# Kernel tuning notes

Measured on AMD Instinct MI355X. Metric: run time of the kernel, lower is better.

Reference implementation:

```python
import jax, jax.numpy as jnp
import numpy as np

B, S, IN, H, D, NH, L, C = 32, 512, 3, 64, 128, 8, 4, 5
NSUB = 10          # euler substeps per interval: dt = interval/10 for these inputs
MAX_CONSEC = 50    # max_consecutive_steps in torch code
DH = D // NH
EPS = 1e-5


def _ln(x, g, b):
    m = x.mean(-1, keepdims=True)
    v = ((x - m) ** 2).mean(-1, keepdims=True)
    return (x - m) / jnp.sqrt(v + EPS) * g + b


def setup_inputs():
    key = jax.random.key(0)
    ks = jax.random.split(key, 24)
    def g(i, shape, scale=0.05):
        return jax.random.normal(ks[i], shape, dtype=jnp.float32) * scale
    dts = jax.random.uniform(ks[0], (B, S), minval=0.001, maxval=0.05, dtype=jnp.float32)
    times = jnp.cumsum(dts, axis=1)  # strictly increasing, positive
    return dict(
        time_series=jax.random.normal(ks[1], (B, S, IN), dtype=jnp.float32),
        times=times,
        noise=jax.random.normal(ks[2], (S, NSUB, B, H), dtype=jnp.float32),
        mask=jnp.ones((B, S), dtype=bool),
        enc_w=g(3, (IN, H)), enc_b=jnp.zeros((H,)),
        enc_g=jnp.ones((H,)), enc_beta=jnp.zeros((H,)),
        dw1=g(4, (H + 1, 2 * H)), db1=jnp.zeros((2 * H,)),
        dw2=g(5, (2 * H, H)), db2=jnp.zeros((H,)),
        dw3=g(6, (H, H)), db3=jnp.zeros((H,)),
        aw1=g(7, (1, H)), ab1=jnp.zeros((H,)),
        aw2=g(8, (H, H)), ab2=jnp.zeros((H,)),
        bw1=g(9, (1, H)), bb1=jnp.zeros((H,)),
        bw2=g(10, (H, H)), bb2=jnp.zeros((H,)),
        min_diff=jnp.float32(0.1),
        in_w=g(11, (H, D)), in_b=jnp.zeros((D,)),
        wq=g(12, (L, D, D)), bq=jnp.zeros((L, D)),
        wk=g(13, (L, D, D)), bk=jnp.zeros((L, D)),
        wv=g(14, (L, D, D)), bv=jnp.zeros((L, D)),
        wo=g(15, (L, D, D)), bo=jnp.zeros((L, D)),
        ln1_g=jnp.ones((L, D)), ln1_b=jnp.zeros((L, D)),
        ln2_g=jnp.ones((L, D)), ln2_b=jnp.zeros((L, D)),
        fw1=g(16, (L, D, 4 * D)), fb1=jnp.zeros((L, 4 * D)),
        fw2=g(17, (L, 4 * D, D)), fb2=jnp.zeros((L, D)),
        cw1=g(18, (D, D // 2)), cb1=jnp.zeros((D // 2,)),
        cw2=g(19, (D // 2, C)), cb2=jnp.zeros((C,)),
    )


def reference(time_series, times, noise, mask, enc_w, enc_b, enc_g, enc_beta,
              dw1, db1, dw2, db2, dw3, db3, aw1, ab1, aw2, ab2, bw1, bb1, bw2, bb2,
              min_diff, in_w, in_b, wq, bq, wk, bk, wv, bv, wo, bo,
              ln1_g, ln1_b, ln2_g, ln2_b, fw1, fb1, fw2, fb2, cw1, cb1, cw2, cb2):
    # feature encoder: Linear -> LayerNorm -> ReLU (dropout off / eval)
    enc = jax.nn.relu(_ln(time_series @ enc_w + enc_b, enc_g, enc_beta))  # (B,S,H)

    def drift(t, y):
        tcol = jnp.full((y.shape[0], 1), t, dtype=y.dtype)
        ty = jnp.concatenate([y, tcol], axis=1)
        h1 = jnp.tanh(ty @ dw1 + db1)
        h2 = jnp.tanh(h1 @ dw2 + db2)
        return h2 @ dw3 + db3

    def diffusion(t, y):
        tcol = jnp.full((y.shape[0], 1), t, dtype=y.dtype)
        A = jax.nn.softplus(jnp.tanh(tcol @ aw1 + ab1) @ aw2 + ab2)
        Bt = jnp.tanh(jnp.tanh(tcol @ bw1 + bb1) @ bw2 + bb2)
        return A + Bt * y + jnp.abs(min_diff)

    t_seq = times[0]  # torch code uses batch element 0's timestamps for sdeint

    def step(carry, xs):
        state, consec = carry
        enc_i, t_prev, t_cur, dW = xs  # dW: (NSUB,B,H) standard normals
        h = (t_cur - t_prev) / NSUB    # dt = interval/10 (< self.dt for these inputs)
        sqh = jnp.sqrt(h)
        y0 = jax.lax.stop_gradient(state)  # torch detaches y0 at every step

        def sub(y, kw):
            k, dw = kw
            t = t_prev + k * h
            return y + drift(t, y) * h + diffusion(t, y) * sqh * dw, None

        y_int, _ = jax.lax.scan(sub, y0, (jnp.arange(NSUB, dtype=jnp.float32), dW))
        skip = consec >= MAX_CONSEC
        out = jnp.where(skip, enc_i, y_int)
        consec = jnp.where(skip, jnp.int32(0), consec + 1)
        return (out, consec), out

    y0 = enc[:, 0]
    xs = (jnp.swapaxes(enc, 0, 1)[1:], t_seq[:-1], t_seq[1:], noise[1:])
    _, traj = jax.lax.scan(step, (y0, jnp.int32(0)), xs)
    sde_features = jnp.concatenate([y0[:, None], jnp.swapaxes(traj, 0, 1)], axis=1)  # (B,S,H)

    mf = mask.astype(sde_features.dtype)
    sde_features = sde_features * mf[..., None]  # MaskedSequenceProcessor.apply_mask

    # ContiFormer (post-LN transformer encoder) over SDE features
    x = sde_features @ in_w + in_b  # (B,S,D)
    neg = jnp.asarray(-1e9, x.dtype)
    for l in range(L):
        q = (x @ wq[l] + bq[l]).reshape(B, S, NH, DH)
        k = (x @ wk[l] + bk[l]).reshape(B, S, NH, DH)
        v = (x @ wv[l] + bv[l]).reshape(B, S, NH, DH)
        scores = jnp.einsum('bqhd,bkhd->bhqk', q, k) / np.float32(np.sqrt(DH))
        scores = jnp.where(mask[:, None, None, :], scores, neg)
        att = jax.nn.softmax(scores, axis=-1)
        o = jnp.einsum('bhqk,bkhd->bqhd', att, v).reshape(B, S, D) @ wo[l] + bo[l]
        x = _ln(x + o, ln1_g[l], ln1_b[l])
        f = jax.nn.relu(x @ fw1[l] + fb1[l]) @ fw2[l] + fb2[l]
        x = _ln(x + f, ln2_g[l], ln2_b[l])
    pooled = (x * mf[..., None]).sum(1) / jnp.maximum(mf.sum(1, keepdims=True), 1.0)

    logits = jax.nn.relu(pooled @ cw1 + cb1) @ cw2 + cb2
    return logits, sde_features
```

## Files before the change

### kernel.cpp

```cpp
#include <hip/hip_runtime.h>
#include <hip/hip_bf16.h>


typedef __attribute__((ext_vector_type(8))) short short8;
typedef __attribute__((ext_vector_type(4))) float f32x4;

static constexpr int OFF_TS      = 0;
static constexpr int OFF_TIMES   = 49152;
static constexpr int OFF_ENCW    = 65536;
static constexpr int OFF_ENCB    = 65728;
static constexpr int OFF_ENCG    = 65792;
static constexpr int OFF_ENCBETA = 65856;
static constexpr int OFF_DW1     = 65920;
static constexpr int OFF_DB1     = 74240;
static constexpr int OFF_DW2     = 74368;
static constexpr int OFF_DB2     = 82560;
static constexpr int OFF_DW3     = 82624;
static constexpr int OFF_DB3     = 86720;
static constexpr int OFF_AW1     = 86784;
static constexpr int OFF_AB1     = 86848;
static constexpr int OFF_AW2     = 86912;
static constexpr int OFF_AB2     = 91008;
static constexpr int OFF_BW1     = 91072;
static constexpr int OFF_BB1     = 91136;
static constexpr int OFF_BW2     = 91200;
static constexpr int OFF_BB2     = 95296;
static constexpr int OFF_MD      = 95360;
static constexpr int OFF_INW     = 95424;
static constexpr int OFF_INB     = 103616;
static constexpr int OFF_WQ      = 103744;
static constexpr int OFF_BQ      = 169280;
static constexpr int OFF_WK      = 169792;
static constexpr int OFF_BK      = 235328;
static constexpr int OFF_WV      = 235840;
static constexpr int OFF_BV      = 301376;
static constexpr int OFF_WO      = 301888;
static constexpr int OFF_BO      = 367424;
static constexpr int OFF_LN1G    = 367936;
static constexpr int OFF_LN1B    = 368448;
static constexpr int OFF_LN2G    = 368960;
static constexpr int OFF_LN2B    = 369472;
static constexpr int OFF_FW1     = 369984;
static constexpr int OFF_FB1     = 632128;
static constexpr int OFF_FW2     = 634176;
static constexpr int OFF_FB2     = 896320;
static constexpr int OFF_CW1     = 896832;
static constexpr int OFF_CB1     = 905024;
static constexpr int OFF_CW2     = 905088;
static constexpr int OFF_CB2     = 905472;
static constexpr int OFF_FLAG    = 905536;
static constexpr int OFF_ENC     = 905600;
static constexpr int OFF_COEFA   = 3002752;
static constexpr int OFF_COEFB   = 3329792;
static constexpr int OFF_B1C     = 3656832;
// ... 278 lines not shown
        c0 = __builtin_amdgcn_mfma_f32_16x16x32_bf16(a0, B1f[0][0], c0, 0, 0, 0);
        c0 = __builtin_amdgcn_mfma_f32_16x16x32_bf16(a1, B1f[1][0], c0, 0, 0, 0);
        f32x4 c1 = {bias_b, bias_b, bias_b, bias_b};
        c1 = __builtin_amdgcn_mfma_f32_16x16x32_bf16(a0, B1f[0][1], c1, 0, 0, 0);
        c1 = __builtin_amdgcn_mfma_f32_16x16x32_bf16(a1, B1f[1][1], c1, 0, 0, 0);
#pragma unroll
        for (int r = 0; r < 4; ++r) {
          h1bf[(q*4 + r)*136 + w*32 + lq]      = f2bf(tanh5(c0[r]));
          h1bf[(q*4 + r)*136 + w*32 + 16 + lq] = f2bf(tanh5(c1[r]));
        }
      }
      lds_barrier();
      {
        short8 h0 = *(const short8*)&h1bf[lq*136 + q*8];
        short8 h1 = *(const short8*)&h1bf[lq*136 + 32 + q*8];
        short8 h2 = *(const short8*)&h1bf[lq*136 + 64 + q*8];
        short8 h3 = *(const short8*)&h1bf[lq*136 + 96 + q*8];
        f32x4 cA = {db2v, db2v, db2v, db2v};
        cA = __builtin_amdgcn_mfma_f32_16x16x32_bf16(h0, B2f[0], cA, 0, 0, 0);
        cA = __builtin_amdgcn_mfma_f32_16x16x32_bf16(h1, B2f[1], cA, 0, 0, 0);
        f32x4 cB = {0.f, 0.f, 0.f, 0.f};
        cB = __builtin_amdgcn_mfma_f32_16x16x32_bf16(h2, B2f[2], cB, 0, 0, 0);
        cB = __builtin_amdgcn_mfma_f32_16x16x32_bf16(h3, B2f[3], cB, 0, 0, 0);
#pragma unroll
        for (int r = 0; r < 4; ++r)
          h2bf[(q*4 + r)*72 + ncol] = f2bf(tanh5(cA[r] + cB[r]));
      }
      lds_barrier();
      {
        short8 g0 = *(const short8*)&h2bf[lq*72 + q*8];
        short8 g1 = *(const short8*)&h2bf[lq*72 + 32 + q*8];
        f32x4 d = {db3v, db3v, db3v, db3v};
        d = __builtin_amdgcn_mfma_f32_16x16x32_bf16(g0, B3f[0], d, 0, 0, 0);
        d = __builtin_amdgcn_mfma_f32_16x16x32_bf16(g1, B3f[1], d, 0, 0, 0);
#pragma unroll
        for (int r = 0; r < 4; ++r) {
          float yv = yreg[r];
          yv = yv + d[r]*hstep + (ca + cb*yv + md)*sqh*dwv[r];
          yreg[r] = yv;
          ybf[(q*4 + r)*72 + ncol] = f2bf(yv);
        }
      }
      bias_a = b1na; bias_b = b1nb; ca = can; cb = cbn;
    }
#pragma unroll
    for (int r = 0; r < 4; ++r) {
      const int gi = ((r0 + q*4 + r)*512 + (istep + 1))*64 + ncol;
      sdebf[gi] = f2bf(yreg[r]);
      outf[160 + gi] = yreg[r];
    }
  }
}

__global__ __launch_bounds__(256) void gemm_ln64_kernel(
    const short* __restrict__ A, const short* __restrict__ BT,
    const float* __restrict__ bias, float* __restrict__ X,
    short* __restrict__ Xb, int K) {
  __shared__ short As[64 * 40];
  __shared__ short Bs[128 * 40];
  const int tid = threadIdx.x;
  const int w = tid >> 6, lane = tid & 63, q = lane >> 4, lq = lane & 15;
  const int bm = blockIdx.x * 64;
  f32x4 acc[8];
#pragma unroll
  for (int i = 0; i < 8; ++i) acc[i] = (f32x4){0.f, 0.f, 0.f, 0.f};

  const int arow = tid >> 2, acol = (tid & 3) * 8;
  const int brow = tid >> 1, bcol = (tid & 1) * 16;
  for (int k0 = 0; k0 < K; k0 += 32) {
    short8 a  = *(const short8*)&A[(bm + arow)*K + k0 + acol];
    short8 b0 = *(const short8*)&BT[brow*K + k0 + bcol];
    short8 b1 = *(const short8*)&BT[brow*K + k0 + bcol + 8];
    __syncthreads();
    *(short8*)&As[arow*40 + acol]    = a;
    *(short8*)&Bs[brow*40 + bcol]    = b0;
    *(short8*)&Bs[brow*40 + bcol+8]  = b1;
    __syncthreads();
    short8 af = *(const short8*)&As[(w*16 + lq)*40 + q*8];
#pragma unroll
    for (int ni = 0; ni < 8; ++ni) {
      short8 bf = *(const short8*)&Bs[(ni*16 + lq)*40 + q*8];
      acc[ni] = __builtin_amdgcn_mfma_f32_16x16x32_bf16(af, bf, acc[ni], 0, 0, 0);
    }
  }
#pragma unroll
  for (int r = 0; r < 4; ++r) {
    const int row = bm + w*16 + q*4 + r;
#pragma unroll
    for (int ni = 0; ni < 8; ++ni) {
      const int col = ni*16 + lq;
      float v = acc[ni][r] + bias[col];
      X[row*128 + col] = v;
      Xb[row*128 + col] = f2bf(v);
    }
  }
}

__global__ __launch_bounds__(512, 2) void ffn_fused_kernel(
    const short* __restrict__ Obf, const short* __restrict__ woT,
    const float* __restrict__ bo,
    const float* __restrict__ ln1g, const float* __restrict__ ln1b,
    const short* __restrict__ fw1T, const float* __restrict__ fb1,
    const short* __restrict__ fw2T, const float* __restrict__ fb2,
    const float* __restrict__ ln2g, const float* __restrict__ ln2b,
    float* __restrict__ X, short* __restrict__ Xb,
    float* __restrict__ psum) {
  __shared__ short U1[64 * 136];
  __shared__ short Hs[64 * 136];
  __shared__ short Bs[128 * 136];
  __shared__ float LNp[64][2][2];
  const int tid = threadIdx.x;
  const int w8 = tid >> 6, rg = w8 & 3, ch = w8 >> 2;
  const int lane = tid & 63, q = lane >> 4, lq = lane & 15;
  const int bm = blockIdx.x * 64;
  const int sr = tid >> 3, sc = (tid & 7) * 16;
  const int bn = tid >> 2, kb = (tid & 3) * 32;
  const int rowl0 = rg*16 + q*4;

  short8 abuf[2], bbuf[4];
#pragma unroll
  for (int j = 0; j < 2; ++j)
    abuf[j] = *(const short8*)&Obf[(bm + sr)*128 + sc + j*8];
#pragma unroll
  for (int j = 0; j < 4; ++j)
    bbuf[j] = *(const short8*)&woT[bn*128 + kb + j*8];
#pragma unroll
  for (int j = 0; j < 2; ++j) *(short8*)&U1[sr*136 + sc + j*8] = abuf[j];
#pragma unroll
  for (int j = 0; j < 4; ++j) *(short8*)&Bs[bn*136 + kb + j*8] = bbuf[j];
  lds_barrier();

#pragma unroll
  for (int j = 0; j < 4; ++j)
    bbuf[j] = *(const short8*)&fw1T[bn*128 + kb + j*8];

  f32x4 acc[4];
#pragma unroll
  for (int i = 0; i < 4; ++i) acc[i] = (f32x4){0.f, 0.f, 0.f, 0.f};
#pragma unroll
  for (int ks = 0; ks < 4; ++ks) {
    short8 af = *(const short8*)&U1[(rg*16 + lq)*136 + ks*32 + q*8];
#pragma unroll
    for (int ni = 0; ni < 4; ++ni) {
      short8 bf = *(const short8*)&Bs[((ch*4 + ni)*16 + lq)*136 + ks*32 + q*8];
      acc[ni] = __builtin_amdgcn_mfma_f32_16x16x32_bf16(af, bf, acc[ni], 0, 0, 0);
    }
  }
  float vbuf[4][4];
#pragma unroll
  for (int r = 0; r < 4; ++r) {
    const int row = bm + rowl0 + r;
    float s = 0.f, s2 = 0.f;
#pragma unroll
    for (int ni = 0; ni < 4; ++ni) {
      const int col = ch*64 + ni*16 + lq;
      float t = acc[ni][r] + bo[col] + X[row*128 + col];
      vbuf[r][ni] = t; s += t; s2 += t*t;
    }
#pragma unroll
    for (int off = 1; off < 16; off <<= 1) {
      s  += __shfl_xor(s, off, 16);
      s2 += __shfl_xor(s2, off, 16);
    }
    if (lq == 0) { LNp[rowl0 + r][ch][0] = s; LNp[rowl0 + r][ch][1] = s2; }
  }
  lds_barrier();
#pragma unroll
  for (int j = 0; j < 4; ++j) *(short8*)&Bs[bn*136 + kb + j*8] = bbuf[j];
#pragma unroll
  for (int j = 0; j < 4; ++j)
    bbuf[j] = *(const short8*)&fw2T[bn*512 + kb + j*8];
  float xv[4][4];
#pragma unroll
  for (int r = 0; r < 4; ++r) {
    const int rowl = rowl0 + r;
    float s  = LNp[rowl][0][0] + LNp[rowl][1][0];
    float s2 = LNp[rowl][0][1] + LNp[rowl][1][1];
    float mean = s * (1.f / 128.f);
    float var = s2 * (1.f / 128.f) - mean * mean;
    float inv = rsqrtf(var + 1e-5f);
#pragma unroll
    for (int ni = 0; ni < 4; ++ni) {
      const int col = ch*64 + ni*16 + lq;
      float o = (vbuf[r][ni] - mean) * inv * ln1g[col] + ln1b[col];
      xv[r][ni] = o;
      U1[rowl*136 + col] = f2bf(o);
    }
  }
  lds_barrier();

  f32x4 acc2[4];
#pragma unroll
  for (int i = 0; i < 4; ++i) acc2[i] = (f32x4){0.f, 0.f, 0.f, 0.f};

  for (int c = 0; c < 4; ++c) {
#pragma unroll
    for (int i = 0; i < 4; ++i) acc[i] = (f32x4){0.f, 0.f, 0.f, 0.f};
#pragma unroll
    for (int ks = 0; ks < 4; ++ks) {
      short8 af = *(const short8*)&U1[(rg*16 + lq)*136 + ks*32 + q*8];
#pragma unroll
      for (int ni = 0; ni < 4; ++ni) {
        short8 bf = *(const short8*)&Bs[((ch*4 + ni)*16 + lq)*136 + ks*32 + q*8];
        acc[ni] = __builtin_amdgcn_mfma_f32_16x16x32_bf16(af, bf, acc[ni], 0, 0, 0);
      }
    }
#pragma unroll
    for (int r = 0; r < 4; ++r)
#pragma unroll
      for (int ni = 0; ni < 4; ++ni) {
        const int cl = ch*64 + ni*16 + lq;
        float hvv = fmaxf(acc[ni][r] + fb1[c*128 + cl], 0.f);
        Hs[(rowl0 + r)*136 + cl] = f2bf(hvv);
      }
    lds_barrier();
#pragma unroll
    for (int j = 0; j < 4; ++j) *(short8*)&Bs[bn*136 + kb + j*8] = bbuf[j];
    if (c < 3) {
#pragma unroll
      for (int j = 0; j < 4; ++j)
        bbuf[j] = *(const short8*)&fw1T[((c + 1)*128 + bn)*128 + kb + j*8];
    }
    lds_barrier();
#pragma unroll
    for (int ks = 0; ks < 4; ++ks) {
      short8 af = *(const short8*)&Hs[(rg*16 + lq)*136 + ks*32 + q*8];
#pragma unroll
      for (int ni = 0; ni < 4; ++ni) {
        short8 bf = *(const short8*)&Bs[((ch*4 + ni)*16 + lq)*136 + ks*32 + q*8];
        acc2[ni] = __builtin_amdgcn_mfma_f32_16x16x32_bf16(af, bf, acc2[ni], 0, 0, 0);
      }
    }
    if (c < 3) {
      lds_barrier();
#pragma unroll
      for (int j = 0; j < 4; ++j) *(short8*)&Bs[bn*136 + kb + j*8] = bbuf[j];
#pragma unroll
      for (int j = 0; j < 4; ++j)
        bbuf[j] = *(const short8*)&fw2T[bn*512 + (c + 1)*128 + kb + j*8];
      lds_barrier();
    }
  }

#pragma unroll
  for (int r = 0; r < 4; ++r) {
    float s = 0.f, s2 = 0.f;
#pragma unroll
    for (int ni = 0; ni < 4; ++ni) {
      const int col = ch*64 + ni*16 + lq;
      float t = acc2[ni][r] + fb2[col] + xv[r][ni];
      vbuf[r][ni] = t; s += t; s2 += t*t;
    }
#pragma unroll
    for (int off = 1; off < 16; off <<= 1) {
      s  += __shfl_xor(s, off, 16);
      s2 += __shfl_xor(s2, off, 16);
    }
    if (lq == 0) { LNp[rowl0 + r][ch][0] = s; LNp[rowl0 + r][ch][1] = s2; }
  }
  lds_barrier();
  float ps[4] = {0.f, 0.f, 0.f, 0.f};
#pragma unroll
  for (int r = 0; r < 4; ++r) {
    const int rowl = rowl0 + r;
    const int row = bm + rowl;
    float s  = LNp[rowl][0][0] + LNp[rowl][1][0];
    float s2 = LNp[rowl][0][1] + LNp[rowl][1][1];
    float mean = s * (1.f / 128.f);
    float var = s2 * (1.f / 128.f) - mean * mean;
    float inv = rsqrtf(var + 1e-5f);
#pragma unroll
    for (int ni = 0; ni < 4; ++ni) {
      const int col = ch*64 + ni*16 + lq;
      float o = (vbuf[r][ni] - mean) * inv * ln2g[col] + ln2b[col];
      X[row*128 + col] = o;
      Xb[row*128 + col] = f2bf(o);
      ps[ni] += o;
    }
  }
  if (psum != nullptr) {
    const int b = bm >> 9;
#pragma unroll
    for (int ni = 0; ni < 4; ++ni) {
      float v = ps[ni];
      v += __shfl_xor(v, 16, 64);
      v += __shfl_xor(v, 32, 64);
      if (q == 0) atomicAdd(&psum[b*128 + ch*64 + ni*16 + lq], v);
    }
  }
}

__global__ __launch_bounds__(512, 2) void attn_fused_kernel(
    const short* __restrict__ Xb, const short* __restrict__ wqkvT,
    const float* __restrict__ bqkv, short* __restrict__ O) {
  __shared__ short Kt[512 * 20];
  __shared__ short Vt[16 * 520];
  __shared__ short U[8 * 2176];
  __shared__ short Qt[8 * 320];
  const int blk = blockIdx.x;
  const int h = blk & 7, b = blk >> 3;
  const int tid = threadIdx.x;
  const int w = tid >> 6, lane = tid & 63, q = lane >> 4, lq = lane & 15;

  short8 BQf[4], BKf[4], BVf[4];
#pragma unroll
  for (int ks = 0; ks < 4; ++ks) {
    BQf[ks] = *(const short8*)&wqkvT[(h*16 + lq)*128 + ks*32 + q*8];
    BKf[ks] = *(const short8*)&wqkvT[(128 + h*16 + lq)*128 + ks*32 + q*8];
    BVf[ks] = *(const short8*)&wqkvT[(256 + h*16 + lq)*128 + ks*32 + q*8];
  }
  const float qb = bqkv[h*16 + lq];
  const float kb = bqkv[128 + h*16 + lq];
  const float vb = bqkv[256 + h*16 + lq];

  short* Uw = &U[w * 2176];
  const int srow = lane >> 2;
  const int scol = (lane & 3) * 32;
  for (int sub = 0; sub < 4; ++sub) {
    const int grow = b*512 + w*64 + sub*16;
    short8 xa[4];
#pragma unroll
    for (int j = 0; j < 4; ++j)
      xa[j] = *(const short8*)&Xb[(size_t)(grow + srow)*128 + scol + j*8];
#pragma unroll
    for (int j = 0; j < 4; ++j)
      *(short8*)&Uw[srow*136 + scol + j*8] = xa[j];
    f32x4 kacc = {0.f, 0.f, 0.f, 0.f};
    f32x4 vacc = {0.f, 0.f, 0.f, 0.f};
#pragma unroll
    for (int ks = 0; ks < 4; ++ks) {
      short8 af = *(const short8*)&Uw[lq*136 + ks*32 + q*8];
      kacc = __builtin_amdgcn_mfma_f32_16x16x32_bf16(af, BKf[ks], kacc, 0, 0, 0);
      vacc = __builtin_amdgcn_mfma_f32_16x16x32_bf16(af, BVf[ks], vacc, 0, 0, 0);
    }
#pragma unroll
    for (int r = 0; r < 4; ++r) {
      const int key = w*64 + sub*16 + q*4 + r;
      Kt[key*20 + lq]  = f2bf(kacc[r] + kb);
      Vt[lq*520 + key] = f2bf(vacc[r] + vb);
    }
  }
  lds_barrier();

  short* Pw = Uw;
  short* Qw = &Qt[w * 320];
  const float cexp = 0.25f * 1.44269504f;

  for (int qi = 0; qi < 4; ++qi) {
    const int qrow0 = b*512 + (w*4 + qi)*16;
    {
      f32x4 qacc = {0.f, 0.f, 0.f, 0.f};
#pragma unroll
      for (int ks = 0; ks < 4; ++ks) {
        short8 af = *(const short8*)&Xb[(size_t)(qrow0 + lq)*128 + ks*32 + q*8];
        qacc = __builtin_amdgcn_mfma_f32_16x16x32_bf16(af, BQf[ks], qacc, 0, 0, 0);
      }
#pragma unroll
      for (int r = 0; r < 4; ++r)
        Qw[(q*4 + r)*20 + lq] = f2bf(qacc[r] + qb);
    }
    short8 aq = (short8){0,0,0,0,0,0,0,0};
    if (q < 2) aq = *(const short8*)&Qw[lq*20 + q*8];

    f32x4 acc[32];
#pragma unroll
    for (int t = 0; t < 32; ++t) {
      short8 bk = (short8){0,0,0,0,0,0,0,0};
      if (q < 2) bk = *(const short8*)&Kt[(t*16 + lq)*20 + q*8];
      f32x4 z = {0.f, 0.f, 0.f, 0.f};
      acc[t] = __builtin_amdgcn_mfma_f32_16x16x32_bf16(aq, bk, z, 0, 0, 0);
    }
    float mx[4] = {-1e30f, -1e30f, -1e30f, -1e30f};
#pragma unroll
    for (int t = 0; t < 32; ++t)
#pragma unroll
      for (int r = 0; r < 4; ++r) mx[r] = fmaxf(mx[r], acc[t][r]);
#pragma unroll
    for (int off = 1; off < 16; off <<= 1)
#pragma unroll
      for (int r = 0; r < 4; ++r) mx[r] = fmaxf(mx[r], __shfl_xor(mx[r], off, 16));
    float ls[4] = {0.f, 0.f, 0.f, 0.f};
#pragma unroll
    for (int t = 0; t < 32; ++t)
#pragma unroll
      for (int r = 0; r < 4; ++r) {
        float p = __builtin_amdgcn_exp2f((acc[t][r] - mx[r]) * cexp);
        acc[t][r] = p;
        ls[r] += p;
      }
#pragma unroll
    for (int off = 1; off < 16; off <<= 1)
#pragma unroll
      for (int r = 0; r < 4; ++r) ls[r] += __shfl_xor(ls[r], off, 16);

    f32x4 o = {0.f, 0.f, 0.f, 0.f};
#pragma unroll
    for (int c = 0; c < 4; ++c) {
#pragma unroll
      for (int tt = 0; tt < 8; ++tt)
#pragma unroll
        for (int r = 0; r < 4; ++r)
          Pw[(q*4 + r)*136 + tt*16 + lq] =
              (short)(__float_as_uint(acc[c*8 + tt][r]) >> 16);
#pragma unroll
      for (int kk = 0; kk < 4; ++kk) {
        short8 ap = *(const short8*)&Pw[lq*136 + kk*32 + q*8];
        short8 bv = *(const short8*)&Vt[lq*520 + c*128 + kk*32 + q*8];
        o = __builtin_amdgcn_mfma_f32_16x16x32_bf16(ap, bv, o, 0, 0, 0);
      }
    }
#pragma unroll
    for (int r = 0; r < 4; ++r) {
      float ov = o[r] * __builtin_amdgcn_rcpf(ls[r]);
      O[(size_t)(qrow0 + q*4 + r)*128 + h*16 + lq] = f2bf(ov);
    }
  }
}

__global__ __launch_bounds__(128) void pool_cls_kernel(const float* __restrict__ W,
                                                       float* __restrict__ outf) {
  int b = blockIdx.x, j = threadIdx.x;
  __shared__ float pooled[128];
  __shared__ float hid[64];
  pooled[j] = W[OFF_TMP + b*128 + j] * (1.f / 512.f);
  __syncthreads();
  if (j < 64) {
    float a = W[OFF_CB1 + j];
    for (int i = 0; i < 128; ++i) a += pooled[i] * W[OFF_CW1 + i*64 + j];
    hid[j] = fmaxf(a, 0.f);
  }
  __syncthreads();
  if (j < 5) {
    float a = W[OFF_CB2 + j];
    for (int i = 0; i < 64; ++i) a += hid[i] * W[OFF_CW2 + i*5 + j];
    outf[b*5 + j] = a;
  }
}

extern "C" void kernel_launch(void* const* d_in, const int* in_sizes, int n_in,
                              void* d_out, int out_size, void* d_ws, size_t ws_size,
                              hipStream_t stream) {
  (void)in_sizes; (void)out_size; (void)ws_size;
  float* W = reinterpret_cast<float*>(d_ws);
  float* outf = reinterpret_cast<float*>(d_out);
  short* sdebf = (short*)(W + OFF_SDEBF);
  short* xbf   = (short*)(W + OFF_XBF);
  short* obf   = (short*)(W + OFF_OBF);
  PtrPack pk;
  for (int i = 0; i < 45 && i < n_in; ++i) pk.p[i] = d_in[i];

  ingest_kernel<<<512, 256, 0, stream>>>(pk, W);
  prelude_kernel<<<5974, 128, 0, stream>>>(W, outf);
  sde_kernel<<<22, 256, 0, stream>>>(W, d_in[2], outf);

  gemm_ln64_kernel<<<256, 256, 0, stream>>>(sdebf, (short*)(W + OFF_INWT),
      W + OFF_INB, W + OFF_X, xbf, 64);
  for (int l = 0; l < 4; ++l) {
    attn_fused_kernel<<<256, 512, 0, stream>>>(xbf,
        (short*)(W + OFF_WQKVT) + l*49152, W + OFF_BQKV + l*384, obf);
    ffn_fused_kernel<<<256, 512, 0, stream>>>(obf,
        (short*)(W + OFF_WOT) + l*16384, W + OFF_BO + l*128,
        W + OFF_LN1G + l*128, W + OFF_LN1B + l*128,
        (short*)(W + OFF_FW1T) + l*65536, W + OFF_FB1 + l*512,
        (short*)(W + OFF_FW2T) + l*65536, W + OFF_FB2 + l*128,
        W + OFF_LN2G + l*128, W + OFF_LN2B + l*128,
        W + OFF_X, xbf, (l == 3) ? (W + OFF_TMP) : nullptr);
  }
  pool_cls_kernel<<<32, 128, 0, stream>>>(W, outf);
}
```

Measured before the change: 865.9 us.

## Merge transformer kernels into one persistent cooperative kernel with grid syncs

Replaces the input GEMM, the per-layer attention and FFN kernels and the pooling classifier with a single cooperative kernel of 256 blocks. Stages are separated by grid.sync plus threadfence, and one shared LDS buffer is reused across stages. This removes about ten kernel launches and their launch gaps. In exchange it pays for grid-wide barriers and needs all 256 blocks of 512 threads to be co-resident.

```diff
diff --git a/kernel.cpp b/kernel.cpp
--- a/kernel.cpp
+++ b/kernel.cpp
@@ -1,5 +1,8 @@
 #include <hip/hip_runtime.h>
 #include <hip/hip_bf16.h>
+#include <hip/hip_cooperative_groups.h>
+
+namespace cg = cooperative_groups;
 
 
 typedef __attribute__((ext_vector_type(8))) short short8;
@@ -384,388 +387,409 @@
   }
 }
 
-__global__ __launch_bounds__(256) void gemm_ln64_kernel(
-    const short* __restrict__ A, const short* __restrict__ BT,
-    const float* __restrict__ bias, float* __restrict__ X,
-    short* __restrict__ Xb, int K) {
-  __shared__ short As[64 * 40];
-  __shared__ short Bs[128 * 40];
+__global__ __launch_bounds__(512, 2) void xformer_kernel(float* __restrict__ W,
+                                                         float* __restrict__ outf) {
+  __shared__ short SM[38528];
+  cg::grid_group grid = cg::this_grid();
+  const int blk = blockIdx.x;
   const int tid = threadIdx.x;
-  const int w = tid >> 6, lane = tid & 63, q = lane >> 4, lq = lane & 15;
-  const int bm = blockIdx.x * 64;
-  f32x4 acc[8];
-#pragma unroll
-  for (int i = 0; i < 8; ++i) acc[i] = (f32x4){0.f, 0.f, 0.f, 0.f};
-
-  const int arow = tid >> 2, acol = (tid & 3) * 8;
-  const int brow = tid >> 1, bcol = (tid & 1) * 16;
-  for (int k0 = 0; k0 < K; k0 += 32) {
-    short8 a  = *(const short8*)&A[(bm + arow)*K + k0 + acol];
-    short8 b0 = *(const short8*)&BT[brow*K + k0 + bcol];
-    short8 b1 = *(const short8*)&BT[brow*K + k0 + bcol + 8];
-    __syncthreads();
-    *(short8*)&As[arow*40 + acol]    = a;
-    *(short8*)&Bs[brow*40 + bcol]    = b0;
-    *(short8*)&Bs[brow*40 + bcol+8]  = b1;
-    __syncthreads();
-    short8 af = *(const short8*)&As[(w*16 + lq)*40 + q*8];
-#pragma unroll
-    for (int ni = 0; ni < 8; ++ni) {
-      short8 bf = *(const short8*)&Bs[(ni*16 + lq)*40 + q*8];
-      acc[ni] = __builtin_amdgcn_mfma_f32_16x16x32_bf16(af, bf, acc[ni], 0, 0, 0);
+  short* sdebf = (short*)(W + OFF_SDEBF);
+  short* xbf   = (short*)(W + OFF_XBF);
+  short* obf   = (short*)(W + OFF_OBF);
+  float* X     = W + OFF_X;
+
+  {
+    short* As = SM;
+    short* Bs = SM + 4608;
+    const short* inwT = (const short*)(W + OFF_INWT);
+    const int w8 = tid >> 6, rg = w8 & 3, cq2 = w8 >> 2;
+    const int lane = tid & 63, q = lane >> 4, lq = lane & 15;
+    const int bm = blk * 64;
+    {
+      const int sr = tid >> 3, sc = (tid & 7) * 8;
+      short8 a = *(const short8*)&sdebf[(bm + sr)*64 + sc];
+      *(short8*)&As[sr*72 + sc] = a;
+    }
+    {
+      const int bn = tid >> 2, kb = (tid & 3) * 16;
+      short8 b0 = *(const short8*)&inwT[bn*64 + kb];
+      short8 b1 = *(const short8*)&inwT[bn*64 + kb + 8];
+      *(short8*)&Bs[bn*72 + kb]     = b0;
+      *(short8*)&Bs[bn*72 + kb + 8] = b1;
+    }
+    lds_barrier();
+    f32x4 acc[4];
+#pragma unroll
+    for (int i = 0; i < 4; ++i) acc[i] = (f32x4){0.f, 0.f, 0.f, 0.f};
+#pragma unroll
+    for (int ks = 0; ks < 2; ++ks) {
+      short8 af = *(const short8*)&As[(rg*16 + lq)*72 + ks*32 + q*8];
+#pragma unroll
+      for (int ni = 0; ni < 4; ++ni) {
+        short8 bf = *(const short8*)&Bs[((cq2*4 + ni)*16 + lq)*72 + ks*32 + q*8];
+        acc[ni] = __builtin_amdgcn_mfma_f32_16x16x32_bf16(af, bf, acc[ni], 0, 0, 0);
+      }
+    }
+#pragma unroll
+    for (int r = 0; r < 4; ++r) {
+      const int row = bm + rg*16 + q*4 + r;
+#pragma unroll
+      for (int ni = 0; ni < 4; ++ni) {
+        const int col = cq2*64 + ni*16 + lq;
+        float v = acc[ni][r] + W[OFF_INB + col];
+        X[row*128 + col] = v;
+        xbf[row*128 + col] = f2bf(v);
+      }
     }
   }
-#pragma unroll
-  for (int r = 0; r < 4; ++r) {
-    const int row = bm + w*16 + q*4 + r;
-#pragma unroll
-    for (int ni = 0; ni < 8; ++ni) {
-      const int col = ni*16 + lq;
-      float v = acc[ni][r] + bias[col];
-      X[row*128 + col] = v;
-      Xb[row*128 + col] = f2bf(v);
-    }
+  __threadfence();
+  grid.sync();
+
+  for (int l = 0; l < 4; ++l) {
+    {
+      short* Kt = SM;
+      short* Vt = SM + 10240;
+      short* U  = SM + 18560;
+      short* Qt = SM + 35968;
+      const short* wqkvT = (const short*)(W + OFF_WQKVT) + l*49152;
+      const float* bqkv = W + OFF_BQKV + l*384;
+      const int h = blk & 7, b = blk >> 3;
+      const int w = tid >> 6, lane = tid & 63, q = lane >> 4, lq = lane & 15;
+
+      short8 BQf[4], BKf[4], BVf[4];
+#pragma unroll
+      for (int ks = 0; ks < 4; ++ks) {
+        BQf[ks] = *(const short8*)&wqkvT[(h*16 + lq)*128 + ks*32 + q*8];
+        BKf[ks] = *(const short8*)&wqkvT[(128 + h*16 + lq)*128 + ks*32 + q*8];
+        BVf[ks] = *(const short8*)&wqkvT[(256 + h*16 + lq)*128 + ks*32 + q*8];
+      }
+      const float qb = bqkv[h*16 + lq];
+      const float kb = bqkv[128 + h*16 + lq];
+      const float vb = bqkv[256 + h*16 + lq];
+
+      short* Uw = &U[w * 2176];
+      const int srow = lane >> 2;
+      const int scol = (lane & 3) * 32;
+      for (int sub = 0; sub < 4; ++sub) {
+        const int grow = b*512 + w*64 + sub*16;
+        short8 xa[4];
+#pragma unroll
+        for (int j = 0; j < 4; ++j)
+          xa[j] = *(const short8*)&xbf[(size_t)(grow + srow)*128 + scol + j*8];
+#pragma unroll
+        for (int j = 0; j < 4; ++j)
+          *(short8*)&Uw[srow*136 + scol + j*8] = xa[j];
+        f32x4 kacc = {0.f, 0.f, 0.f, 0.f};
+        f32x4 vacc = {0.f, 0.f, 0.f, 0.f};
+#pragma unroll
+        for (int ks = 0; ks < 4; ++ks) {
+          short8 af = *(const short8*)&Uw[lq*136 + ks*32 + q*8];
+          kacc = __builtin_amdgcn_mfma_f32_16x16x32_bf16(af, BKf[ks], kacc, 0, 0, 0);
+          vacc = __builtin_amdgcn_mfma_f32_16x16x32_bf16(af, BVf[ks], vacc, 0, 0, 0);
+        }
+#pragma unroll
+        for (int r = 0; r < 4; ++r) {
+          const int key = w*64 + sub*16 + q*4 + r;
+          Kt[key*20 + lq]  = f2bf(kacc[r] + kb);
+          Vt[lq*520 + key] = f2bf(vacc[r] + vb);
+        }
+      }
+      lds_barrier();
+
+      short* Pw = Uw;
+      short* Qw = &Qt[w * 320];
+      const float cexp = 0.25f * 1.44269504f;
+
+      for (int qi = 0; qi < 4; ++qi) {
+        const int qrow0 = b*512 + (w*4 + qi)*16;
+        {
+          f32x4 qacc = {0.f, 0.f, 0.f, 0.f};
+#pragma unroll
+          for (int ks = 0; ks < 4; ++ks) {
+            short8 af = *(const short8*)&xbf[(size_t)(qrow0 + lq)*128 + ks*32 + q*8];
+            qacc = __builtin_amdgcn_mfma_f32_16x16x32_bf16(af, BQf[ks], qacc, 0, 0, 0);
+          }
+#pragma unroll
+          for (int r = 0; r < 4; ++r)
+            Qw[(q*4 + r)*20 + lq] = f2bf(qacc[r] + qb);
+        }
+        short8 aq = (short8){0,0,0,0,0,0,0,0};
+        if (q < 2) aq = *(const short8*)&Qw[lq*20 + q*8];
+
+        f32x4 acc[32];
+#pragma unroll
+        for (int t = 0; t < 32; ++t) {
+          short8 bk = (short8){0,0,0,0,0,0,0,0};
+          if (q < 2) bk = *(const short8*)&Kt[(t*16 + lq)*20 + q*8];
+          f32x4 z = {0.f, 0.f, 0.f, 0.f};
+          acc[t] = __builtin_amdgcn_mfma_f32_16x16x32_bf16(aq, bk, z, 0, 0, 0);
+        }
+        float mx[4] = {-1e30f, -1e30f, -1e30f, -1e30f};
+#pragma unroll
+        for (int t = 0; t < 32; ++t)
+#pragma unroll
+          for (int r = 0; r < 4; ++r) mx[r] = fmaxf(mx[r], acc[t][r]);
+#pragma unroll
+        for (int off = 1; off < 16; off <<= 1)
+#pragma unroll
+          for (int r = 0; r < 4; ++r) mx[r] = fmaxf(mx[r], __shfl_xor(mx[r], off, 16));
+        float ls[4] = {0.f, 0.f, 0.f, 0.f};
+#pragma unroll
+        for (int t = 0; t < 32; ++t)
+#pragma unroll
+          for (int r = 0; r < 4; ++r) {
+            float p = __builtin_amdgcn_exp2f((acc[t][r] - mx[r]) * cexp);
+            acc[t][r] = p;
+            ls[r] += p;
+          }
+#pragma unroll
+        for (int off = 1; off < 16; off <<= 1)
+#pragma unroll
+          for (int r = 0; r < 4; ++r) ls[r] += __shfl_xor(ls[r], off, 16);
+
+        f32x4 o = {0.f, 0.f, 0.f, 0.f};
+#pragma unroll
+        for (int c = 0; c < 4; ++c) {
+#pragma unroll
+          for (int tt = 0; tt < 8; ++tt)
+#pragma unroll
+            for (int r = 0; r < 4; ++r)
+              Pw[(q*4 + r)*136 + tt*16 + lq] =
+                  (short)(__float_as_uint(acc[c*8 + tt][r]) >> 16);
+#pragma unroll
+          for (int kk = 0; kk < 4; ++kk) {
+            short8 ap = *(const short8*)&Pw[lq*136 + kk*32 + q*8];
+            short8 bv = *(const short8*)&Vt[lq*520 + c*128 + kk*32 + q*8];
+            o = __builtin_amdgcn_mfma_f32_16x16x32_bf16(ap, bv, o, 0, 0, 0);
+          }
+        }
+#pragma unroll
+        for (int r = 0; r < 4; ++r) {
+          float ov = o[r] * __builtin_amdgcn_rcpf(ls[r]);
+          obf[(size_t)(qrow0 + q*4 + r)*128 + h*16 + lq] = f2bf(ov);
+        }
+      }
+    }
+    __threadfence();
+    grid.sync();
+
+    {
+      short* U1  = SM;
+      short* Hs  = SM + 8704;
+      short* Bsf = SM + 17408;
+      float* LNp = (float*)(SM + 34816);
+      const short* woT  = (const short*)(W + OFF_WOT) + l*16384;
+      const float* bo   = W + OFF_BO + l*128;
+      const float* ln1g = W + OFF_LN1G + l*128;
+      const float* ln1b = W + OFF_LN1B + l*128;
+      const short* fw1T = (const short*)(W + OFF_FW1T) + l*65536;
+      const float* fb1  = W + OFF_FB1 + l*512;
+      const short* fw2T = (const short*)(W + OFF_FW2T) + l*65536;
+      const float* fb2  = W + OFF_FB2 + l*128;
+      const float* ln2g = W + OFF_LN2G + l*128;
+      const float* ln2b = W + OFF_LN2B + l*128;
+      float* psum = (l == 3) ? (W + OFF_TMP) : nullptr;
+      const int w8 = tid >> 6, rg = w8 & 3, ch = w8 >> 2;
+      const int lane = tid & 63, q = lane >> 4, lq = lane & 15;
+      const int bm = blk * 64;
+      const int sr = tid >> 3, sc = (tid & 7) * 16;
+      const int bn = tid >> 2, kb = (tid & 3) * 32;
+      const int rowl0 = rg*16 + q*4;
+
+      short8 abuf[2], bbuf[4];
+#pragma unroll
+      for (int j = 0; j < 2; ++j)
+        abuf[j] = *(const short8*)&obf[(bm + sr)*128 + sc + j*8];
+#pragma unroll
+      for (int j = 0; j < 4; ++j)
+        bbuf[j] = *(const short8*)&woT[bn*128 + kb + j*8];
+#pragma unroll
+      for (int j = 0; j < 2; ++j) *(short8*)&U1[sr*136 + sc + j*8] = abuf[j];
+#pragma unroll
+      for (int j = 0; j < 4; ++j) *(short8*)&Bsf[bn*136 + kb + j*8] = bbuf[j];
+      lds_barrier();
+
+#pragma unroll
+      for (int j = 0; j < 4; ++j)
+        bbuf[j] = *(const short8*)&fw1T[bn*128 + kb + j*8];
+
+      f32x4 acc[4];
+#pragma unroll
+      for (int i = 0; i < 4; ++i) acc[i] = (f32x4){0.f, 0.f, 0.f, 0.f};
+#pragma unroll
+      for (int ks = 0; ks < 4; ++ks) {
+        short8 af = *(const short8*)&U1[(rg*16 + lq)*136 + ks*32 + q*8];
+#pragma unroll
+        for (int ni = 0; ni < 4; ++ni) {
+          short8 bf = *(const short8*)&Bsf[((ch*4 + ni)*16 + lq)*136 + ks*32 + q*8];
+          acc[ni] = __builtin_amdgcn_mfma_f32_16x16x32_bf16(af, bf, acc[ni], 0, 0, 0);
+        }
+      }
+      float vbuf[4][4];
+#pragma unroll
+      for (int r = 0; r < 4; ++r) {
+        const int row = bm + rowl0 + r;
+        float s = 0.f, s2 = 0.f;
+#pragma unroll
+        for (int ni = 0; ni < 4; ++ni) {
+          const int col = ch*64 + ni*16 + lq;
+          float t = acc[ni][r] + bo[col] + X[row*128 + col];
+          vbuf[r][ni] = t; s += t; s2 += t*t;
+        }
+#pragma unroll
+        for (int off = 1; off < 16; off <<= 1) {
+          s  += __shfl_xor(s, off, 16);
+          s2 += __shfl_xor(s2, off, 16);
+        }
+        if (lq == 0) { LNp[(rowl0 + r)*4 + ch*2 + 0] = s; LNp[(rowl0 + r)*4 + ch*2 + 1] = s2; }
+      }
+      lds_barrier();
+#pragma unroll
+      for (int j = 0; j < 4; ++j) *(short8*)&Bsf[bn*136 + kb + j*8] = bbuf[j];
+#pragma unroll
+      for (int j = 0; j < 4; ++j)
+        bbuf[j] = *(const short8*)&fw2T[bn*512 + kb + j*8];
+      float xv[4][4];
+#pragma unroll
+      for (int r = 0; r < 4; ++r) {
+        const int rowl = rowl0 + r;
+        float s  = LNp[rowl*4 + 0] + LNp[rowl*4 + 2];
+        float s2 = LNp[rowl*4 + 1] + LNp[rowl*4 + 3];
+        float mean = s * (1.f / 128.f);
+        float var = s2 * (1.f / 128.f) - mean * mean;
+        float inv = rsqrtf(var + 1e-5f);
+#pragma unroll
+        for (int ni = 0; ni < 4; ++ni) {
+          const int col = ch*64 + ni*16 + lq;
+          float o = (vbuf[r][ni] - mean) * inv * ln1g[col] + ln1b[col];
+          xv[r][ni] = o;
+          U1[rowl*136 + col] = f2bf(o);
+        }
+      }
+      lds_barrier();
+
+      f32x4 acc2[4];
+#pragma unroll
+      for (int i = 0; i < 4; ++i) acc2[i] = (f32x4){0.f, 0.f, 0.f, 0.f};
+
+      for (int c = 0; c < 4; ++c) {
+#pragma unroll
+        for (int i = 0; i < 4; ++i) acc[i] = (f32x4){0.f, 0.f, 0.f, 0.f};
+#pragma unroll
+        for (int ks = 0; ks < 4; ++ks) {
+          short8 af = *(const short8*)&U1[(rg*16 + lq)*136 + ks*32 + q*8];
+#pragma unroll
+          for (int ni = 0; ni < 4; ++ni) {
+            short8 bf = *(const short8*)&Bsf[((ch*4 + ni)*16 + lq)*136 + ks*32 + q*8];
+            acc[ni] = __builtin_amdgcn_mfma_f32_16x16x32_bf16(af, bf, acc[ni], 0, 0, 0);
+          }
+        }
+#pragma unroll
+        for (int r = 0; r < 4; ++r)
+#pragma unroll
+          for (int ni = 0; ni < 4; ++ni) {
+            float hvv = fmaxf(acc[ni][r] + fb1[c*128 + ch*64 + ni*16 + lq], 0.f);
+            Hs[(rowl0 + r)*136 + ch*64 + ni*16 + lq] = f2bf(hvv);
+          }
+        lds_barrier();
+#pragma unroll
+        for (int j = 0; j < 4; ++j) *(short8*)&Bsf[bn*136 + kb + j*8] = bbuf[j];
+        if (c < 3) {
+#pragma unroll
+          for (int j = 0; j < 4; ++j)
+            bbuf[j] = *(const short8*)&fw1T[((c + 1)*128 + bn)*128 + kb + j*8];
+        }
+        lds_barrier();
+#pragma unroll
+        for (int ks = 0; ks < 4; ++ks) {
+          short8 af = *(const short8*)&Hs[(rg*16 + lq)*136 + ks*32 + q*8];
+#pragma unroll
+          for (int ni = 0; ni < 4; ++ni) {
+            short8 bf = *(const short8*)&Bsf[((ch*4 + ni)*16 + lq)*136 + ks*32 + q*8];
+            acc2[ni] = __builtin_amdgcn_mfma_f32_16x16x32_bf16(af, bf, acc2[ni], 0, 0, 0);
+          }
+        }
+        if (c < 3) {
+          lds_barrier();
+#pragma unroll
+          for (int j = 0; j < 4; ++j) *(short8*)&Bsf[bn*136 + kb + j*8] = bbuf[j];
+#pragma unroll
+          for (int j = 0; j < 4; ++j)
+            bbuf[j] = *(const short8*)&fw2T[bn*512 + (c + 1)*128 + kb + j*8];
+          lds_barrier();
+        }
+      }
+
+      float ps[4];
+#pragma unroll
+      for (int ni = 0; ni < 4; ++ni) ps[ni] = 0.f;
+      lds_barrier();
+#pragma unroll
+      for (int r = 0; r < 4; ++r) {
+        float s = 0.f, s2 = 0.f;
+#pragma unroll
+        for (int ni = 0; ni < 4; ++ni) {
+          const int col = ch*64 + ni*16 + lq;
+          float t = acc2[ni][r] + fb2[col] + xv[r][ni];
+          vbuf[r][ni] = t; s += t; s2 += t*t;
+        }
+#pragma unroll
+        for (int off = 1; off < 16; off <<= 1) {
+          s  += __shfl_xor(s, off, 16);
+          s2 += __shfl_xor(s2, off, 16);
+        }
+        if (lq == 0) { LNp[(rowl0 + r)*4 + ch*2 + 0] = s; LNp[(rowl0 + r)*4 + ch*2 + 1] = s2; }
+      }
+      lds_barrier();
+#pragma unroll
+      for (int r = 0; r < 4; ++r) {
+        const int rowl = rowl0 + r;
+        const int row = bm + rowl;
+        float s  = LNp[rowl*4 + 0] + LNp[rowl*4 + 2];
+        float s2 = LNp[rowl*4 + 1] + LNp[rowl*4 + 3];
+        float mean = s * (1.f / 128.f);
+        float var = s2 * (1.f / 128.f) - mean * mean;
+        float inv = rsqrtf(var + 1e-5f);
+#pragma unroll
+        for (int ni = 0; ni < 4; ++ni) {
+          const int col = ch*64 + ni*16 + lq;
+          float o = (vbuf[r][ni] - mean) * inv * ln2g[col] + ln2b[col];
+          X[row*128 + col] = o;
+          xbf[row*128 + col] = f2bf(o);
+          ps[ni] += o;
+        }
+      }
+      if (psum != nullptr) {
+        const int b2 = bm >> 9;
+#pragma unroll
+        for (int ni = 0; ni < 4; ++ni) {
+          float v = ps[ni];
+          v += __shfl_xor(v, 16, 64);
+          v += __shfl_xor(v, 32, 64);
+          if (q == 0) atomicAdd(&psum[b2*128 + ch*64 + ni*16 + lq], v);
+        }
+      }
+    }
+    __threadfence();
+    grid.sync();
   }
-}
-
-__global__ __launch_bounds__(512, 2) void ffn_fused_kernel(
-    const short* __restrict__ Obf, const short* __restrict__ woT,
-    const float* __restrict__ bo,
-    const float* __restrict__ ln1g, const float* __restrict__ ln1b,
-    const short* __restrict__ fw1T, const float* __restrict__ fb1,
-    const short* __restrict__ fw2T, const float* __restrict__ fb2,
-    const float* __restrict__ ln2g, const float* __restrict__ ln2b,
-    float* __restrict__ X, short* __restrict__ Xb,
-    float* __restrict__ psum) {
-  __shared__ short U1[64 * 136];
-  __shared__ short Hs[64 * 136];
-  __shared__ short Bs[128 * 136];
-  __shared__ float LNp[64][2][2];
-  const int tid = threadIdx.x;
-  const int w8 = tid >> 6, rg = w8 & 3, ch = w8 >> 2;
-  const int lane = tid & 63, q = lane >> 4, lq = lane & 15;
-  const int bm = blockIdx.x * 64;
-  const int sr = tid >> 3, sc = (tid & 7) * 16;
-  const int bn = tid >> 2, kb = (tid & 3) * 32;
-  const int rowl0 = rg*16 + q*4;
-
-  short8 abuf[2], bbuf[4];
-#pragma unroll
-  for (int j = 0; j < 2; ++j)
-    abuf[j] = *(const short8*)&Obf[(bm + sr)*128 + sc + j*8];
-#pragma unroll
-  for (int j = 0; j < 4; ++j)
-    bbuf[j] = *(const short8*)&woT[bn*128 + kb + j*8];
-#pragma unroll
-  for (int j = 0; j < 2; ++j) *(short8*)&U1[sr*136 + sc + j*8] = abuf[j];
-#pragma unroll
-  for (int j = 0; j < 4; ++j) *(short8*)&Bs[bn*136 + kb + j*8] = bbuf[j];
-  lds_barrier();
-
-#pragma unroll
-  for (int j = 0; j < 4; ++j)
-    bbuf[j] = *(const short8*)&fw1T[bn*128 + kb + j*8];
-
-  f32x4 acc[4];
-#pragma unroll
-  for (int i = 0; i < 4; ++i) acc[i] = (f32x4){0.f, 0.f, 0.f, 0.f};
-#pragma unroll
-  for (int ks = 0; ks < 4; ++ks) {
-    short8 af = *(const short8*)&U1[(rg*16 + lq)*136 + ks*32 + q*8];
-#pragma unroll
-    for (int ni = 0; ni < 4; ++ni) {
-      short8 bf = *(const short8*)&Bs[((ch*4 + ni)*16 + lq)*136 + ks*32 + q*8];
-      acc[ni] = __builtin_amdgcn_mfma_f32_16x16x32_bf16(af, bf, acc[ni], 0, 0, 0);
-    }
-  }
-  float vbuf[4][4];
-#pragma unroll
-  for (int r = 0; r < 4; ++r) {
-    const int row = bm + rowl0 + r;
-    float s = 0.f, s2 = 0.f;
-#pragma unroll
-    for (int ni = 0; ni < 4; ++ni) {
-      const int col = ch*64 + ni*16 + lq;
-      float t = acc[ni][r] + bo[col] + X[row*128 + col];
-      vbuf[r][ni] = t; s += t; s2 += t*t;
-    }
-#pragma unroll
-    for (int off = 1; off < 16; off <<= 1) {
-      s  += __shfl_xor(s, off, 16);
-      s2 += __shfl_xor(s2, off, 16);
-    }
-    if (lq == 0) { LNp[rowl0 + r][ch][0] = s; LNp[rowl0 + r][ch][1] = s2; }
-  }
-  lds_barrier();
-#pragma unroll
-  for (int j = 0; j < 4; ++j) *(short8*)&Bs[bn*136 + kb + j*8] = bbuf[j];
-#pragma unroll
-  for (int j = 0; j < 4; ++j)
-    bbuf[j] = *(const short8*)&fw2T[bn*512 + kb + j*8];
-  float xv[4][4];
-#pragma unroll
-  for (int r = 0; r < 4; ++r) {
-    const int rowl = rowl0 + r;
-    float s  = LNp[rowl][0][0] + LNp[rowl][1][0];
-    float s2 = LNp[rowl][0][1] + LNp[rowl][1][1];
-    float mean = s * (1.f / 128.f);
-    float var = s2 * (1.f / 128.f) - mean * mean;
-    float inv = rsqrtf(var + 1e-5f);
-#pragma unroll
-    for (int ni = 0; ni < 4; ++ni) {
-      const int col = ch*64 + ni*16 + lq;
-      float o = (vbuf[r][ni] - mean) * inv * ln1g[col] + ln1b[col];
-      xv[r][ni] = o;
-      U1[rowl*136 + col] = f2bf(o);
-    }
-  }
-  lds_barrier();
-
-  f32x4 acc2[4];
-#pragma unroll
-  for (int i = 0; i < 4; ++i) acc2[i] = (f32x4){0.f, 0.f, 0.f, 0.f};
-
-  for (int c = 0; c < 4; ++c) {
-#pragma unroll
-    for (int i = 0; i < 4; ++i) acc[i] = (f32x4){0.f, 0.f, 0.f, 0.f};
-#pragma unroll
-    for (int ks = 0; ks < 4; ++ks) {
-      short8 af = *(const short8*)&U1[(rg*16 + lq)*136 + ks*32 + q*8];
-#pragma unroll
-      for (int ni = 0; ni < 4; ++ni) {
-        short8 bf = *(const short8*)&Bs[((ch*4 + ni)*16 + lq)*136 + ks*32 + q*8];
-        acc[ni] = __builtin_amdgcn_mfma_f32_16x16x32_bf16(af, bf, acc[ni], 0, 0, 0);
-      }
-    }
-#pragma unroll
-    for (int r = 0; r < 4; ++r)
-#pragma unroll
-      for (int ni = 0; ni < 4; ++ni) {
-        const int cl = ch*64 + ni*16 + lq;
-        float hvv = fmaxf(acc[ni][r] + fb1[c*128 + cl], 0.f);
-        Hs[(rowl0 + r)*136 + cl] = f2bf(hvv);
-      }
+
+  if (blk < 32) {
+    float* pooled = (float*)SM;
+    float* hid    = (float*)SM + 128;
+    if (tid < 128) pooled[tid] = W[OFF_TMP + blk*128 + tid] * (1.f / 512.f);
     lds_barrier();
-#pragma unroll
-    for (int j = 0; j < 4; ++j) *(short8*)&Bs[bn*136 + kb + j*8] = bbuf[j];
-    if (c < 3) {
-#pragma unroll
-      for (int j = 0; j < 4; ++j)
-        bbuf[j] = *(const short8*)&fw1T[((c + 1)*128 + bn)*128 + kb + j*8];
+    if (tid < 64) {
+      float a = W[OFF_CB1 + tid];
+      for (int i = 0; i < 128; ++i) a += pooled[i] * W[OFF_CW1 + i*64 + tid];
+      hid[tid] = fmaxf(a, 0.f);
     }
     lds_barrier();
-#pragma unroll
-    for (int ks = 0; ks < 4; ++ks) {
-      short8 af = *(const short8*)&Hs[(rg*16 + lq)*136 + ks*32 + q*8];
-#pragma unroll
-      for (int ni = 0; ni < 4; ++ni) {
-        short8 bf = *(const short8*)&Bs[((ch*4 + ni)*16 + lq)*136 + ks*32 + q*8];
-        acc2[ni] = __builtin_amdgcn_mfma_f32_16x16x32_bf16(af, bf, acc2[ni], 0, 0, 0);
-      }
-    }
-    if (c < 3) {
-      lds_barrier();
-#pragma unroll
-      for (int j = 0; j < 4; ++j) *(short8*)&Bs[bn*136 + kb + j*8] = bbuf[j];
-#pragma unroll
-      for (int j = 0; j < 4; ++j)
-        bbuf[j] = *(const short8*)&fw2T[bn*512 + (c + 1)*128 + kb + j*8];
-      lds_barrier();
-    }
-  }
-
-#pragma unroll
-  for (int r = 0; r < 4; ++r) {
-    float s = 0.f, s2 = 0.f;
-#pragma unroll
-    for (int ni = 0; ni < 4; ++ni) {
-      const int col = ch*64 + ni*16 + lq;
-      float t = acc2[ni][r] + fb2[col] + xv[r][ni];
-      vbuf[r][ni] = t; s += t; s2 += t*t;
-    }
-#pragma unroll
-    for (int off = 1; off < 16; off <<= 1) {
-      s  += __shfl_xor(s, off, 16);
-      s2 += __shfl_xor(s2, off, 16);
-    }
-    if (lq == 0) { LNp[rowl0 + r][ch][0] = s; LNp[rowl0 + r][ch][1] = s2; }
-  }
-  lds_barrier();
-  float ps[4] = {0.f, 0.f, 0.f, 0.f};
-#pragma unroll
-  for (int r = 0; r < 4; ++r) {
-    const int rowl = rowl0 + r;
-    const int row = bm + rowl;
-    float s  = LNp[rowl][0][0] + LNp[rowl][1][0];
-    float s2 = LNp[rowl][0][1] + LNp[rowl][1][1];
-    float mean = s * (1.f / 128.f);
-    float var = s2 * (1.f / 128.f) - mean * mean;
-    float inv = rsqrtf(var + 1e-5f);
-#pragma unroll
-    for (int ni = 0; ni < 4; ++ni) {
-      const int col = ch*64 + ni*16 + lq;
-      float o = (vbuf[r][ni] - mean) * inv * ln2g[col] + ln2b[col];
-      X[row*128 + col] = o;
-      Xb[row*128 + col] = f2bf(o);
-      ps[ni] += o;
-    }
-  }
-  if (psum != nullptr) {
-    const int b = bm >> 9;
-#pragma unroll
-    for (int ni = 0; ni < 4; ++ni) {
-      float v = ps[ni];
-      v += __shfl_xor(v, 16, 64);
-      v += __shfl_xor(v, 32, 64);
-      if (q == 0) atomicAdd(&psum[b*128 + ch*64 + ni*16 + lq], v);
-    }
-  }
-}
-
-__global__ __launch_bounds__(512, 2) void attn_fused_kernel(
-    const short* __restrict__ Xb, const short* __restrict__ wqkvT,
-    const float* __restrict__ bqkv, short* __restrict__ O) {
-  __shared__ short Kt[512 * 20];
-  __shared__ short Vt[16 * 520];
-  __shared__ short U[8 * 2176];
-  __shared__ short Qt[8 * 320];
-  const int blk = blockIdx.x;
-  const int h = blk & 7, b = blk >> 3;
-  const int tid = threadIdx.x;
-  const int w = tid >> 6, lane = tid & 63, q = lane >> 4, lq = lane & 15;
-
-  short8 BQf[4], BKf[4], BVf[4];
-#pragma unroll
-  for (int ks = 0; ks < 4; ++ks) {
-    BQf[ks] = *(const short8*)&wqkvT[(h*16 + lq)*128 + ks*32 + q*8];
-    BKf[ks] = *(const short8*)&wqkvT[(128 + h*16 + lq)*128 + ks*32 + q*8];
-    BVf[ks] = *(const short8*)&wqkvT[(256 + h*16 + lq)*128 + ks*32 + q*8];
-  }
-  const float qb = bqkv[h*16 + lq];
-  const float kb = bqkv[128 + h*16 + lq];
-  const float vb = bqkv[256 + h*16 + lq];
-
-  short* Uw = &U[w * 2176];
-  const int srow = lane >> 2;
-  const int scol = (lane & 3) * 32;
-  for (int sub = 0; sub < 4; ++sub) {
-    const int grow = b*512 + w*64 + sub*16;
-    short8 xa[4];
-#pragma unroll
-    for (int j = 0; j < 4; ++j)
-      xa[j] = *(const short8*)&Xb[(size_t)(grow + srow)*128 + scol + j*8];
-#pragma unroll
-    for (int j = 0; j < 4; ++j)
-      *(short8*)&Uw[srow*136 + scol + j*8] = xa[j];
-    f32x4 kacc = {0.f, 0.f, 0.f, 0.f};
-    f32x4 vacc = {0.f, 0.f, 0.f, 0.f};
-#pragma unroll
-    for (int ks = 0; ks < 4; ++ks) {
-      short8 af = *(const short8*)&Uw[lq*136 + ks*32 + q*8];
-      kacc = __builtin_amdgcn_mfma_f32_16x16x32_bf16(af, BKf[ks], kacc, 0, 0, 0);
-      vacc = __builtin_amdgcn_mfma_f32_16x16x32_bf16(af, BVf[ks], vacc, 0, 0, 0);
-    }
-#pragma unroll
-    for (int r = 0; r < 4; ++r) {
-      const int key = w*64 + sub*16 + q*4 + r;
-      Kt[key*20 + lq]  = f2bf(kacc[r] + kb);
-      Vt[lq*520 + key] = f2bf(vacc[r] + vb);
-    }
-  }
-  lds_barrier();
-
-  short* Pw = Uw;
-  short* Qw = &Qt[w * 320];
-  const float cexp = 0.25f * 1.44269504f;
-
-  for (int qi = 0; qi < 4; ++qi) {
-    const int qrow0 = b*512 + (w*4 + qi)*16;
-    {
-      f32x4 qacc = {0.f, 0.f, 0.f, 0.f};
-#pragma unroll
-      for (int ks = 0; ks < 4; ++ks) {
-        short8 af = *(const short8*)&Xb[(size_t)(qrow0 + lq)*128 + ks*32 + q*8];
-        qacc = __builtin_amdgcn_mfma_f32_16x16x32_bf16(af, BQf[ks], qacc, 0, 0, 0);
-      }
-#pragma unroll
-      for (int r = 0; r < 4; ++r)
-        Qw[(q*4 + r)*20 + lq] = f2bf(qacc[r] + qb);
-    }
-    short8 aq = (short8){0,0,0,0,0,0,0,0};
-    if (q < 2) aq = *(const short8*)&Qw[lq*20 + q*8];
-
-    f32x4 acc[32];
-#pragma unroll
-    for (int t = 0; t < 32; ++t) {
-      short8 bk = (short8){0,0,0,0,0,0,0,0};
-      if (q < 2) bk = *(const short8*)&Kt[(t*16 + lq)*20 + q*8];
-      f32x4 z = {0.f, 0.f, 0.f, 0.f};
-      acc[t] = __builtin_amdgcn_mfma_f32_16x16x32_bf16(aq, bk, z, 0, 0, 0);
-    }
-    float mx[4] = {-1e30f, -1e30f, -1e30f, -1e30f};
-#pragma unroll
-    for (int t = 0; t < 32; ++t)
-#pragma unroll
-      for (int r = 0; r < 4; ++r) mx[r] = fmaxf(mx[r], acc[t][r]);
-#pragma unroll
-    for (int off = 1; off < 16; off <<= 1)
-#pragma unroll
-      for (int r = 0; r < 4; ++r) mx[r] = fmaxf(mx[r], __shfl_xor(mx[r], off, 16));
-    float ls[4] = {0.f, 0.f, 0.f, 0.f};
-#pragma unroll
-    for (int t = 0; t < 32; ++t)
-#pragma unroll
-      for (int r = 0; r < 4; ++r) {
-        float p = __builtin_amdgcn_exp2f((acc[t][r] - mx[r]) * cexp);
-        acc[t][r] = p;
-        ls[r] += p;
-      }
-#pragma unroll
-    for (int off = 1; off < 16; off <<= 1)
-#pragma unroll
-      for (int r = 0; r < 4; ++r) ls[r] += __shfl_xor(ls[r], off, 16);
-
-    f32x4 o = {0.f, 0.f, 0.f, 0.f};
-#pragma unroll
-    for (int c = 0; c < 4; ++c) {
-#pragma unroll
-      for (int tt = 0; tt < 8; ++tt)
-#pragma unroll
-        for (int r = 0; r < 4; ++r)
-          Pw[(q*4 + r)*136 + tt*16 + lq] =
-              (short)(__float_as_uint(acc[c*8 + tt][r]) >> 16);
-#pragma unroll
-      for (int kk = 0; kk < 4; ++kk) {
-        short8 ap = *(const short8*)&Pw[lq*136 + kk*32 + q*8];
-        short8 bv = *(const short8*)&Vt[lq*520 + c*128 + kk*32 + q*8];
-        o = __builtin_amdgcn_mfma_f32_16x16x32_bf16(ap, bv, o, 0, 0, 0);
-      }
-    }
-#pragma unroll
-    for (int r = 0; r < 4; ++r) {
-      float ov = o[r] * __builtin_amdgcn_rcpf(ls[r]);
-      O[(size_t)(qrow0 + q*4 + r)*128 + h*16 + lq] = f2bf(ov);
-    }
-  }
-}
-
-__global__ __launch_bounds__(128) void pool_cls_kernel(const float* __restrict__ W,
-                                                       float* __restrict__ outf) {
-  int b = blockIdx.x, j = threadIdx.x;
-  __shared__ float pooled[128];
-  __shared__ float hid[64];
-  pooled[j] = W[OFF_TMP + b*128 + j] * (1.f / 512.f);
-  __syncthreads();
-  if (j < 64) {
-    float a = W[OFF_CB1 + j];
-    for (int i = 0; i < 128; ++i) a += pooled[i] * W[OFF_CW1 + i*64 + j];
-    hid[j] = fmaxf(a, 0.f);
-  }
-  __syncthreads();
-  if (j < 5) {
-    float a = W[OFF_CB2 + j];
-    for (int i = 0; i < 64; ++i) a += hid[i] * W[OFF_CW2 + i*5 + j];
-    outf[b*5 + j] = a;
+    if (tid < 5) {
+      float a = W[OFF_CB2 + tid];
+      for (int i = 0; i < 64; ++i) a += hid[i] * W[OFF_CW2 + i*5 + tid];
+      outf[blk*5 + tid] = a;
+    }
   }
 }
 
@@ -775,9 +799,6 @@
   (void)in_sizes; (void)out_size; (void)ws_size;
   float* W = reinterpret_cast<float*>(d_ws);
   float* outf = reinterpret_cast<float*>(d_out);
-  short* sdebf = (short*)(W + OFF_SDEBF);
-  short* xbf   = (short*)(W + OFF_XBF);
-  short* obf   = (short*)(W + OFF_OBF);
   PtrPack pk;
   for (int i = 0; i < 45 && i < n_in; ++i) pk.p[i] = d_in[i];
 
@@ -785,18 +806,8 @@
   prelude_kernel<<<5974, 128, 0, stream>>>(W, outf);
   sde_kernel<<<22, 256, 0, stream>>>(W, d_in[2], outf);
 
-  gemm_ln64_kernel<<<256, 256, 0, stream>>>(sdebf, (short*)(W + OFF_INWT),
-      W + OFF_INB, W + OFF_X, xbf, 64);
-  for (int l = 0; l < 4; ++l) {
-    attn_fused_kernel<<<256, 512, 0, stream>>>(xbf,
-        (short*)(W + OFF_WQKVT) + l*49152, W + OFF_BQKV + l*384, obf);
-    ffn_fused_kernel<<<256, 512, 0, stream>>>(obf,
-        (short*)(W + OFF_WOT) + l*16384, W + OFF_BO + l*128,
-        W + OFF_LN1G + l*128, W + OFF_LN1B + l*128,
-        (short*)(W + OFF_FW1T) + l*65536, W + OFF_FB1 + l*512,
-        (short*)(W + OFF_FW2T) + l*65536, W + OFF_FB2 + l*128,
-        W + OFF_LN2G + l*128, W + OFF_LN2B + l*128,
-        W + OFF_X, xbf, (l == 3) ? (W + OFF_TMP) : nullptr);
-  }
-  pool_cls_kernel<<<32, 128, 0, stream>>>(W, outf);
-}
+  void* kargs[2];
+  kargs[0] = (void*)&W;
+  kargs[1] = (void*)&outf;
+  hipLaunchCooperativeKernel(xformer_kernel, dim3(256), dim3(512), kargs, 0u, stream);
+}
```

Result: slower. 1.689 ms (+95.1%).
